# Kernel tuning notes

Hardware: AMD Instinct MI355X
Metric: run time of the kernel (lower is better)

The kernel has to match this reference:

```python
import jax, jax.numpy as jnp
import numpy as np

K = 10
EPS = 1e-5  # BatchNorm eps, eval mode with running_mean=0, running_var=1


def mish(x):
    return x * jnp.tanh(jax.nn.softplus(x))


def knn_idx(x, k):
    # x: (B, C, N); returns (B, N, k) indices of k nearest neighbors (incl. self)
    xx = jnp.sum(x * x, axis=1)                      # (B, N)
    inner = jnp.einsum('bcn,bcm->bnm', x, x)         # (B, N, N)
    neg_d = 2.0 * inner - xx[:, :, None] - xx[:, None, :]
    return jax.lax.top_k(neg_d, k)[1]


def graph_feature(x, k):
    # x: (B, C, N) -> edge features (B, 2C, N, k): cat(nbr - x, x)
    idx = knn_idx(x, k)
    x_t = jnp.transpose(x, (0, 2, 1))                # (B, N, C)
    nbr = jax.vmap(lambda xt, ix: xt[ix])(x_t, idx)  # (B, N, k, C)
    ctr = jnp.broadcast_to(x_t[:, :, None, :], nbr.shape)
    edge = jnp.concatenate([nbr - ctr, ctr], axis=-1)
    return jnp.transpose(edge, (0, 3, 1, 2))


def block2d(x, W, g, b):
    # Conv2d(kernel=1, bias=False) + BatchNorm2d(eval) + Mish
    y = jnp.einsum('oi,bink->bonk', W, x)
    y = y * (g / jnp.sqrt(1.0 + EPS))[None, :, None, None] + b[None, :, None, None]
    return mish(y)


def block1d(x, W, g, b):
    # Conv1d(kernel=1, bias=False) + BatchNorm1d(eval) + Mish
    y = jnp.einsum('oi,bin->bon', W, x)
    y = y * (g / jnp.sqrt(1.0 + EPS))[None, :, None] + b[None, :, None]
    return mish(y)


def setup_inputs() -> dict:
    key = jax.random.key(0)
    ks = jax.random.split(key, 32)
    B, N = 8, 4096
    x = jax.random.normal(ks[0], (B, 3, N), dtype=jnp.float32)

    def w(k, o, i):
        return jax.random.normal(k, (o, i), dtype=jnp.float32) * np.float32(np.sqrt(2.0 / i))

    W1 = w(ks[1], 64, 6)
    W2 = w(ks[2], 64, 128)
    W3 = w(ks[3], 128, 128)
    W4 = w(ks[4], 128, 128)
    W5 = w(ks[5], 128, 256)
    W6 = w(ks[6], 64, 128)
    W7 = w(ks[7], 64, 128)
    W8 = w(ks[8], 64, 128)
    W9 = w(ks[9], 2, 64)

    bn_sizes = [64, 64, 128, 128, 128, 64, 64, 64]
    gs, bs = [], []
    for i, c in enumerate(bn_sizes):
        gs.append(1.0 + 0.1 * jax.random.normal(ks[10 + i], (c,), dtype=jnp.float32))
        bs.append(0.1 * jax.random.normal(ks[20 + i], (c,), dtype=jnp.float32))

    d = {'x': x, 'W1': W1, 'W2': W2, 'W3': W3, 'W4': W4, 'W5': W5,
         'W6': W6, 'W7': W7, 'W8': W8, 'W9': W9}
    for i in range(8):
        d['g%d' % (i + 1)] = gs[i]
        d['b%d' % (i + 1)] = bs[i]
    return d


def reference(x, W1, W2, W3, W4, W5, W6, W7, W8, W9,
              g1, g2, g3, g4, g5, g6, g7, g8,
              b1, b2, b3, b4, b5, b6, b7, b8):
    e = graph_feature(x, K)                      # (B, 6, N, k)
    x1 = jnp.max(block2d(e, W1, g1, b1), axis=-1)  # (B, 64, N)
    e = graph_feature(x1, K)                     # (B, 128, N, k)
    x2 = jnp.max(block2d(e, W2, g2, b2), axis=-1)  # (B, 64, N)
    e = graph_feature(x2, K)                     # (B, 128, N, k)
    x3 = jnp.max(block2d(e, W3, g3, b3), axis=-1)  # (B, 128, N)
    h = block1d(x3, W4, g4, b4)                  # (B, 128, N)
    h = block1d(jnp.concatenate([h, x3], axis=1), W5, g5, b5)  # (B, 128, N)
    h = block1d(h, W6, g6, b6)                   # (B, 64, N)
    h = block1d(jnp.concatenate([h, x2], axis=1), W7, g7, b7)  # (B, 64, N)
    h = block1d(jnp.concatenate([h, x1], axis=1), W8, g8, b8)  # (B, 64, N)
    return jnp.einsum('oi,bin->bon', W9, h)      # (B, 2, N)
```

## Files before the change

kernel.cpp:

```cpp
#include <hip/hip_runtime.h>
#include <hip/hip_bf16.h>
#include <math.h>
#include <float.h>

#define B_ 8
#define N_ 4096
#define M_ (B_*N_)
#define KNN 10

typedef unsigned long long ull;
typedef __attribute__((ext_vector_type(8))) short s16x8;
typedef __attribute__((ext_vector_type(4))) float f32x4;

__device__ __forceinline__ float mishf(float x){
  float sp = (x > 20.f) ? x : __logf(1.f + __expf(x));
  float e2 = __expf(-2.f*sp);
  float th = (1.f - e2) / (1.f + e2);
  return x * th;
}

__device__ __forceinline__ ull shfl_xor_u64(ull v, int mask){
  unsigned lo = (unsigned)v, hi = (unsigned)(v >> 32);
  lo = (unsigned)__shfl_xor((int)lo, mask);
  hi = (unsigned)__shfl_xor((int)hi, mask);
  return ((ull)hi << 32) | lo;
}
__device__ __forceinline__ ull shfl_u64(ull v, int src){
  unsigned lo = (unsigned)v, hi = (unsigned)(v >> 32);
  lo = (unsigned)__shfl((int)lo, src);
  hi = (unsigned)__shfl((int)hi, src);
  return ((ull)hi << 32) | lo;
}
__device__ __forceinline__ int mbcnt_lt(ull mask){
  return __builtin_amdgcn_mbcnt_hi((unsigned)(mask>>32),
         __builtin_amdgcn_mbcnt_lo((unsigned)mask, 0));
}
__device__ __forceinline__ unsigned mono_u32(float f){
  unsigned u = __float_as_uint(f);
  return u ^ ((unsigned)((int)u >> 31) | 0x80000000u);
}
__device__ __forceinline__ float unmono(unsigned vk){
  unsigned u = (vk & 0x80000000u) ? (vk ^ 0x80000000u) : ~vk;
  return __uint_as_float(u);
}
__device__ __forceinline__ void gload_lds16(const void* g, void* l){
  __builtin_amdgcn_global_load_lds(
      (const __attribute__((address_space(1))) unsigned int*)g,
      (__attribute__((address_space(3))) unsigned int*)l, 16, 0, 0);
}

__global__ __launch_bounds__(256) void k_transpose_x(const float* __restrict__ x,
                                                     float* __restrict__ xp){
  int n = blockIdx.x*256 + threadIdx.x;
  if (n >= M_) return;
  int b = n >> 12, i = n & (N_-1);
  const float* xb = x + (size_t)b*3*N_;
  float v0 = xb[i], v1 = xb[N_+i], v2 = xb[2*N_+i];
  float* o = xp + (size_t)n*3;
  o[0]=v0; o[1]=v1; o[2]=v2;
}

template<int C>
__global__ __launch_bounds__(256) void k_xx(const float* __restrict__ X,
                                            float* __restrict__ xx){
  int n = blockIdx.x*256 + threadIdx.x;
  if (n >= M_) return;
  const float* r = X + (size_t)n*C;
  float s = 0.f;
#pragma unroll
  for (int c=0;c<C;c++){ float v=r[c]; s = fmaf(v,v,s); }
  xx[n] = s;
}

__global__ __launch_bounds__(256) void k_cvt(const float* __restrict__ X,
                                             ushort* __restrict__ Xhi,
                                             ushort* __restrict__ Xlo){
  int i = blockIdx.x*256 + threadIdx.x;
  const float4* src = (const float4*)X + (size_t)i*2;
  float4 v0 = src[0], v1 = src[1];
  float vv[8] = {v0.x,v0.y,v0.z,v0.w,v1.x,v1.y,v1.z,v1.w};
  ushort h[8], l[8];
#pragma unroll
  for (int e=0;e<8;e++){
    __hip_bfloat16 hb = __float2bfloat16(vv[e]);
    float hf = __bfloat162float(hb);
    __hip_bfloat16 lb = __float2bfloat16(vv[e]-hf);
    h[e] = *(ushort*)&hb; l[e] = *(ushort*)&lb;
  }
  uint4 hp, lp;
  hp.x = (unsigned)h[0] | ((unsigned)h[1]<<16);
  hp.y = (unsigned)h[2] | ((unsigned)h[3]<<16);
  hp.z = (unsigned)h[4] | ((unsigned)h[5]<<16);
  hp.w = (unsigned)h[6] | ((unsigned)h[7]<<16);
  lp.x = (unsigned)l[0] | ((unsigned)l[1]<<16);
  lp.y = (unsigned)l[2] | ((unsigned)l[3]<<16);
  lp.z = (unsigned)l[4] | ((unsigned)l[5]<<16);
  lp.w = (unsigned)l[6] | ((unsigned)l[7]<<16);
  *(uint4*)(Xhi + (size_t)i*8) = hp;
  *(uint4*)(Xlo + (size_t)i*8) = lp;
}

__global__ __launch_bounds__(256,2) void k_knn64m(const ushort* __restrict__ Xhi,
                                                  const ushort* __restrict__ Xlo,
                                                  const float* __restrict__ xx,
                                                  int* __restrict__ idxout){
  constexpr int JT  = 128;
  constexpr int NT  = N_/JT;
  constexpr int CAP = 320;
  __shared__ ushort XJhi[2][JT*64];
  __shared__ ushort XJlo[2][JT*64];
  __shared__ float  halfxx[2][JT];
  __shared__ ull    buf[4][CAP];

  const int t    = threadIdx.x;
  const int w    = t >> 6;
  const int lane = t & 63;
  const int b    = blockIdx.x & 7;
  const int i0   = (blockIdx.x >> 3) * 64;
  const size_t rowbase = (size_t)b*N_;
  const float* xxb = xx + rowbase;

  const int arow = i0 + w*16 + (lane & 15);
  const ushort* Ah = Xhi + (rowbase + arow)*64;
  const ushort* Al = Xlo + (rowbase + arow)*64;
  const int ko = (lane >> 4)*8;
  s16x8 aH0 = *(const s16x8*)(Ah + ko);
  s16x8 aH1 = *(const s16x8*)(Ah + 32 + ko);
  s16x8 aL0 = *(const s16x8*)(Al + ko);
  s16x8 aL1 = *(const s16x8*)(Al + 32 + ko);

  ull kq[KNN];
#pragma unroll
  for (int q=0;q<KNN;q++) kq[q]=0ull;
  float Treg = -INFINITY;

  const int lr = lane >> 3;
  const int sc = (lane & 7) ^ lr;

  {
#pragma unroll
    for (int seg=0; seg<4; ++seg){
      const int row0 = w*32 + seg*8;
      gload_lds16(Xhi + (rowbase + row0 + lr)*64 + sc*8, &XJhi[0][row0*64]);
      gload_lds16(Xlo + (rowbase + row0 + lr)*64 + sc*8, &XJlo[0][row0*64]);
    }
    if (t < JT) halfxx[0][t] = 0.5f*xxb[t];
  }
  __syncthreads();

  for (int jt = 0; jt < NT; ++jt){
    const int cur = jt & 1;
    const int j0 = jt*JT;

    float hnext = 0.f;
    if (jt < NT-1){
      const size_t nb0 = rowbase + j0 + JT;
#pragma unroll
      for (int seg=0; seg<4; ++seg){
        const int row0 = w*32 + seg*8;
        gload_lds16(Xhi + (nb0 + row0 + lr)*64 + sc*8, &XJhi[cur^1][row0*64]);
        gload_lds16(Xlo + (nb0 + row0 + lr)*64 + sc*8, &XJlo[cur^1][row0*64]);
      }
      if (t < JT) hnext = 0.5f*xxb[j0 + JT + t];
    }

    f32x4 acc[8];
#pragma unroll
    for (int cb=0;cb<8;cb++) acc[cb] = (f32x4){0.f,0.f,0.f,0.f};

#pragma unroll
    for (int cb=0;cb<8;cb++){
      const int brow = cb*16 + (lane & 15);
      const unsigned sw = ((unsigned)(brow & 7)) << 4;
      const char* ph = (const char*)&XJhi[cur][0] + brow*128;
      const char* pl = (const char*)&XJlo[cur][0] + brow*128;
      const int kb0 = (int)((unsigned)((lane>>4)<<4) ^ sw);
      const int kb1 = (int)((unsigned)(64 | ((lane>>4)<<4)) ^ sw);
      s16x8 bh0 = *(const s16x8*)(ph + kb0);
      s16x8 bl0 = *(const s16x8*)(pl + kb0);
      s16x8 bh1 = *(const s16x8*)(ph + kb1);
      s16x8 bl1 = *(const s16x8*)(pl + kb1);
      f32x4 a = acc[cb];
      a = __builtin_amdgcn_mfma_f32_16x16x32_bf16(aH0, bh0, a, 0,0,0);
      a = __builtin_amdgcn_mfma_f32_16x16x32_bf16(aH0, bl0, a, 0,0,0);
      a = __builtin_amdgcn_mfma_f32_16x16x32_bf16(aL0, bh0, a, 0,0,0);
      a = __builtin_amdgcn_mfma_f32_16x16x32_bf16(aL0, bl0, a, 0,0,0);
      a = __builtin_amdgcn_mfma_f32_16x16x32_bf16(aH1, bh1, a, 0,0,0);
      a = __builtin_amdgcn_mfma_f32_16x16x32_bf16(aH1, bl1, a, 0,0,0);
      a = __builtin_amdgcn_mfma_f32_16x16x32_bf16(aL1, bh1, a, 0,0,0);
      a = __builtin_amdgcn_mfma_f32_16x16x32_bf16(aL1, bl1, a, 0,0,0);
      acc[cb] = a;
    }

    float hx[8];
#pragma unroll
    for (int cb=0;cb<8;cb++) hx[cb] = halfxx[cur][cb*16 + (lane & 15)];

    if (jt < NT-1 && t < JT) halfxx[cur^1][t] = hnext;

    if (jt == 0){
#pragma unroll
      for (int reg=0;reg<4;reg++){
        const unsigned rl = (unsigned)((lane>>4)*4 + reg);
        ull k8[8];
#pragma unroll
        for (int cb=0;cb<8;cb++){
          float v = acc[cb][reg] - hx[cb];
          unsigned jinv = 4095u - (unsigned)(cb*16 + (lane & 15));
          k8[cb] = ((ull)mono_u32(v)<<32) | ((ull)jinv<<4) | rl;
        }
#pragma unroll
        for (int q=0;q<KNN;q++){
          ull m = k8[0];
#pragma unroll
          for (int s=1;s<8;s++) m = m > k8[s] ? m : k8[s];
          ull v1 = shfl_xor_u64(m,1); m = m>v1?m:v1;
          ull v2 = shfl_xor_u64(m,2); m = m>v2?m:v2;
          ull v4 = shfl_xor_u64(m,4); m = m>v4?m:v4;
          ull v8 = shfl_xor_u64(m,8); m = m>v8?m:v8;
          ull mv = shfl_u64(m, (lane>>2)<<4);
          if (lane < 16 && (lane&3)==reg) kq[q] = mv;
#pragma unroll
          for (int s=0;s<8;s++) k8[s] = (k8[s]==m) ? 0ull : k8[s];
        }
      }
      Treg = unmono((unsigned)(kq[KNN-1] >> 32));
    } else {
      float Tf[4];
#pragma unroll
      for (int reg=0;reg<4;reg++) Tf[reg] = __shfl(Treg, (lane>>4)*4 + reg);
      int cnt = 0;
#pragma unroll
      for (int cb=0;cb<8;cb++){
#pragma unroll
        for (int reg=0;reg<4;reg++){
          float v = acc[cb][reg] - hx[cb];
          bool pass = v >= Tf[reg];
          ull mask = __ballot(pass);
          if (mask){
            if (pass){
              int slot = cnt + mbcnt_lt(mask);
              unsigned jinv = 4095u - (unsigned)(j0 + cb*16 + (lane & 15));
              ull key = ((ull)mono_u32(v)<<32) | ((ull)jinv<<4)
                        | (unsigned)((lane>>4)*4 + reg);
              if (slot < CAP) buf[w][slot] = key;
            }
            cnt += __popcll(mask);
          }
        }
      }
      if (cnt){
        int nb = cnt < CAP ? cnt : CAP;
        int pad = (4 - (nb & 3)) & 3;
        if (lane < pad && nb + lane < CAP) buf[w][nb + lane] = 0ull;
        int nb4 = nb + pad; if (nb4 > CAP) nb4 = CAP;
        for (int e=0;e<nb4;e+=4){
          ull c0=buf[w][e+0], c1=buf[w][e+1], c2=buf[w][e+2], c3=buf[w][e+3];
#pragma unroll
          for (int u=0;u<4;u++){
            ull k64 = (u==0)?c0:(u==1)?c1:(u==2)?c2:c3;
            if ((int)(k64 & 15ull) == lane && k64 > kq[KNN-1]){
              ull ck = k64;
#pragma unroll
              for (int q=0;q<KNN;q++){
                ull hi = ck > kq[q] ? ck : kq[q];
                ull lo = ck > kq[q] ? kq[q] : ck;
                kq[q] = hi; ck = lo;
              }
            }
          }
        }
        Treg = unmono((unsigned)(kq[KNN-1] >> 32));
      }
    }
    __syncthreads();
  }

  if (lane < 16){
    int* o = idxout + ((size_t)b*N_ + i0 + w*16 + lane)*KNN;
#pragma unroll
    for (int q=0;q<KNN;q++) o[q] = (int)(4095u - (unsigned)((kq[q]>>4) & 4095ull));
  }
}

template<int C>
__global__ __launch_bounds__(256,2) void k_knn(const float* __restrict__ X,
                                               const float* __restrict__ xx,
                                               int* __restrict__ idxout){
  constexpr bool BIG = (C % 4 == 0);
  constexpr int LS  = BIG ? (C + 4) : 12;
  constexpr int NC4 = BIG ? (C/4 + 1) : 1;
  constexpr int JT  = 128;
  constexpr int CAP = 320;
  __shared__ float XI[64*LS];
  __shared__ float XJ[JT*LS];
  __shared__ ull   buf[4][CAP];

  const int t    = threadIdx.x;
  const int w    = t >> 6;
  const int lane = t & 63;
  const int b    = blockIdx.y;
  const int i0   = blockIdx.x*64;
  const int tc   = t & 15, tr = t >> 4;
  const float* Xb  = X  + (size_t)b*N_*C;
  const float* xxb = xx + (size_t)b*N_;

  if constexpr (BIG){
    for (int f = t; f < 64*(C/4); f += 256){
      int r = f >> 4, c4 = f & 15;
      *(float4*)&XI[r*LS + c4*4] = *(const float4*)&Xb[(size_t)(i0+r)*C + c4*4];
    }
    if (t < 64){ XI[t*LS+C]=1.f; XI[t*LS+C+1]=0.f; XI[t*LS+C+2]=0.f; XI[t*LS+C+3]=0.f; }
  } else {
    if (t < 64){
      const float* p = &Xb[(size_t)(i0+t)*C];
      XI[t*LS+0]=p[0]; XI[t*LS+1]=p[1]; XI[t*LS+2]=p[2]; XI[t*LS+3]=1.f;
    }
  }

  ull kq[KNN];
#pragma unroll
  for (int q=0;q<KNN;q++) kq[q]=0ull;
  float Treg = -INFINITY;

  for (int jt = 0; jt < N_/JT; ++jt){
    const int j0 = jt*JT;
    if constexpr (BIG){
      for (int f = t; f < JT*(C/4); f += 256){
        int r = f >> 4, c4 = f & 15;
        *(float4*)&XJ[r*LS + c4*4] = *(const float4*)&Xb[(size_t)(j0+r)*C + c4*4];
      }
      if (t < JT){ XJ[t*LS+C] = -0.5f*xxb[j0+t]; XJ[t*LS+C+1]=0.f; XJ[t*LS+C+2]=0.f; XJ[t*LS+C+3]=0.f; }
    } else {
      if (t < JT){
        const float* p = &Xb[(size_t)(j0+t)*C];
        XJ[t*LS+0]=p[0]; XJ[t*LS+1]=p[1]; XJ[t*LS+2]=p[2]; XJ[t*LS+3]=-0.5f*xxb[j0+t];
      }
    }
    __syncthreads();

    float acc[4][8];
#pragma unroll
    for (int rr=0;rr<4;rr++)
#pragma unroll
      for (int s=0;s<8;s++) acc[rr][s]=0.f;

#pragma unroll 2
    for (int c4 = 0; c4 < NC4; ++c4){
      float4 xi0 = *(const float4*)&XI[(tr*4+0)*LS + c4*4];
      float4 xi1 = *(const float4*)&XI[(tr*4+1)*LS + c4*4];
      float4 xi2 = *(const float4*)&XI[(tr*4+2)*LS + c4*4];
      float4 xi3 = *(const float4*)&XI[(tr*4+3)*LS + c4*4];
#pragma unroll
      for (int s=0;s<8;s++){
        float4 xj = *(const float4*)&XJ[(tc+16*s)*LS + c4*4];
        float a0=acc[0][s], a1=acc[1][s], a2=acc[2][s], a3=acc[3][s];
        a0=fmaf(xi0.x,xj.x,a0); a1=fmaf(xi1.x,xj.x,a1); a2=fmaf(xi2.x,xj.x,a2); a3=fmaf(xi3.x,xj.x,a3);
        a0=fmaf(xi0.y,xj.y,a0); a1=fmaf(xi1.y,xj.y,a1); a2=fmaf(xi2.y,xj.y,a2); a3=fmaf(xi3.y,xj.y,a3);
        a0=fmaf(xi0.z,xj.z,a0); a1=fmaf(xi1.z,xj.z,a1); a2=fmaf(xi2.z,xj.z,a2); a3=fmaf(xi3.z,xj.z,a3);
        a0=fmaf(xi0.w,xj.w,a0); a1=fmaf(xi1.w,xj.w,a1); a2=fmaf(xi2.w,xj.w,a2); a3=fmaf(xi3.w,xj.w,a3);
        acc[0][s]=a0; acc[1][s]=a1; acc[2][s]=a2; acc[3][s]=a3;
      }
    }

    if (jt == 0){
#pragma unroll
      for (int rr=0;rr<4;rr++){
        const unsigned rl = (unsigned)((lane>>4)*4 + rr);
        ull k8[8];
#pragma unroll
        for (int s=0;s<8;s++){
          unsigned jinv = 4095u - (unsigned)(tc + 16*s);
          k8[s] = ((ull)mono_u32(acc[rr][s])<<32) | ((ull)jinv<<4) | rl;
        }
#pragma unroll
        for (int q=0;q<KNN;q++){
          ull m = k8[0];
#pragma unroll
          for (int s=1;s<8;s++) m = m > k8[s] ? m : k8[s];
          ull v1 = shfl_xor_u64(m,1); m = m>v1?m:v1;
          ull v2 = shfl_xor_u64(m,2); m = m>v2?m:v2;
          ull v4 = shfl_xor_u64(m,4); m = m>v4?m:v4;
          ull v8 = shfl_xor_u64(m,8); m = m>v8?m:v8;
          ull mv = shfl_u64(m, (lane>>2)<<4);
          if (lane < 16 && (lane&3)==rr) kq[q] = mv;
#pragma unroll
          for (int s=0;s<8;s++) k8[s] = (k8[s]==m) ? 0ull : k8[s];
        }
      }
      Treg = unmono((unsigned)(kq[KNN-1] >> 32));
    } else {
      float Tf[4];
#pragma unroll
      for (int rr=0;rr<4;rr++) Tf[rr] = __shfl(Treg, (lane>>4)*4 + rr);
      int cnt = 0;
#pragma unroll
      for (int s=0;s<8;s++){
#pragma unroll
        for (int rr=0;rr<4;rr++){
          bool pass = acc[rr][s] >= Tf[rr];
          ull mask = __ballot(pass);
          if (mask){
            if (pass){
              int slot = cnt + mbcnt_lt(mask);
              unsigned jinv = 4095u - (unsigned)(j0 + tc + 16*s);
              ull key = ((ull)mono_u32(acc[rr][s])<<32) | ((ull)jinv<<4)
                        | (unsigned)((lane>>4)*4 + rr);
              if (slot < CAP) buf[w][slot] = key;
            }
            cnt += __popcll(mask);
          }
        }
      }
      if (cnt){
        int nb = cnt < CAP ? cnt : CAP;
        for (int e=0;e<nb;e++){
          ull k64 = buf[w][e];
          if ((int)(k64 & 15ull) == lane && k64 > kq[KNN-1]){
            ull ck = k64;
#pragma unroll
            for (int q=0;q<KNN;q++){
              ull hi = ck > kq[q] ? ck : kq[q];
              ull lo = ck > kq[q] ? kq[q] : ck;
              kq[q] = hi; ck = lo;
            }
          }
        }
        Treg = unmono((unsigned)(kq[KNN-1] >> 32));
      }
    }
    __syncthreads();
  }

  if (lane < 16){
    int* o = idxout + ((size_t)b*N_ + i0 + w*16 + lane)*KNN;
#pragma unroll
    for (int q=0;q<KNN;q++) o[q] = (int)(4095u - (unsigned)((kq[q]>>4) & 4095ull));
  }
}

template<int PT>
__global__ __launch_bounds__(256) void k_gemm(
    const float* __restrict__ X1, int C1,
    const float* __restrict__ X2, int C2,
    const float* __restrict__ W, int hmask, int hshift, int wstride, int hoff,
    const float* __restrict__ g, const float* __restrict__ bb, int act,
    float* __restrict__ Y, int Pfull)
{
  constexpr int CPT = PT/16;
  constexpr int WLS = PT + 4;
  __shared__ float Xt[32*68];
  __shared__ float Wt[32*WLS];
  const int t  = threadIdx.x;
  const int r0 = blockIdx.x*64;
  const int p0 = blockIdx.y*PT;
  const int cg = t & 15, rg = t >> 4;
  const int C = C1 + C2;
  const int nkt = (C + 31) >> 5;

  float acc[4][CPT];
#pragma unroll
  for (int a=0;a<4;a++)
#pragma unroll
    for (int c=0;c<CPT;c++) acc[a][c]=0.f;

  for (int kt = 0; kt < nkt; ++kt){
    const int k0 = kt*32;
#pragma unroll
    for (int e = t; e < 64*32; e += 256){
      int kk = e & 31, r = e >> 5;
      int gk = k0 + kk;
      float v = 0.f;
      if (gk < C1) v = X1[(size_t)(r0+r)*C1 + gk];
      else if (gk < C) v = X2[(size_t)(r0+r)*C2 + (gk - C1)];
      Xt[kk*68 + r] = v;
    }
#pragma unroll
    for (int e = t; e < PT*32; e += 256){
      int kk = e & 31, p = e >> 5;
      int gp = p0 + p;
      int wrow = (gp & hmask)*wstride + (gp >> hshift)*hoff;
      int gk = k0 + kk;
      Wt[kk*WLS + p] = (gk < C) ? W[(size_t)wrow + gk] : 0.f;
    }
    __syncthreads();
#pragma unroll
    for (int kk=0;kk<32;kk++){
      float4 xv = *(const float4*)&Xt[kk*68 + rg*4];
      float xr[4] = {xv.x, xv.y, xv.z, xv.w};
      float wv[CPT];
#pragma unroll
      for (int c4=0;c4<CPT/4;c4++){
        float4 w4 = *(const float4*)&Wt[kk*WLS + cg*CPT + c4*4];
        wv[c4*4+0]=w4.x; wv[c4*4+1]=w4.y; wv[c4*4+2]=w4.z; wv[c4*4+3]=w4.w;
      }
#pragma unroll
      for (int rr=0;rr<4;rr++)
#pragma unroll
        for (int cc=0;cc<CPT;cc++)
          acc[rr][cc] = fmaf(xr[rr], wv[cc], acc[rr][cc]);
    }
    __syncthreads();
  }

  const float srs = rsqrtf(1.f + 1e-5f);
  float sv[CPT], bvv[CPT];
#pragma unroll
  for (int cc=0;cc<CPT;cc++){
    int gp = p0 + cg*CPT + cc;
    if (g){ sv[cc] = g[gp]*srs; bvv[cc] = bb[gp]; } else { sv[cc]=1.f; bvv[cc]=0.f; }
  }
#pragma unroll
  for (int rr=0;rr<4;rr++){
    size_t row = r0 + rg*4 + rr;
    float* yr = Y + row*(size_t)Pfull + p0 + cg*CPT;
#pragma unroll
    for (int c4=0;c4<CPT/4;c4++){
      float y0 = sv[c4*4+0]*acc[rr][c4*4+0] + bvv[c4*4+0];
      float y1 = sv[c4*4+1]*acc[rr][c4*4+1] + bvv[c4*4+1];
      float y2 = sv[c4*4+2]*acc[rr][c4*4+2] + bvv[c4*4+2];
      float y3 = sv[c4*4+3]*acc[rr][c4*4+3] + bvv[c4*4+3];
      if (act){ y0=mishf(y0); y1=mishf(y1); y2=mishf(y2); y3=mishf(y3); }
      *(float4*)&yr[c4*4] = make_float4(y0,y1,y2,y3);
    }
  }
}

template<int O>
__global__ __launch_bounds__(256) void k_edgemax(
    const float* __restrict__ ua, const int* __restrict__ idx,
    const float* __restrict__ g, const float* __restrict__ bb,
    float* __restrict__ Y)
{
  constexpr int TPR = O/4;
  const int gt = blockIdx.x*256 + threadIdx.x;
  const int m  = gt / TPR;
  const int og = gt % TPR;
  if (m >= M_) return;
  const int base = m & ~(N_-1);
  const int P = 2*O;
  const float4 u0 = *(const float4*)&ua[(size_t)m*P + og*4];
  const float4 a0 = *(const float4*)&ua[(size_t)m*P + O + og*4];
  const float srs = rsqrtf(1.f + 1e-5f);
  const float4 gv  = *(const float4*)&g[og*4];
  const float4 bv4 = *(const float4*)&bb[og*4];
  const float sx = gv.x*srs, sy = gv.y*srs, sz = gv.z*srs, sw = gv.w*srs;
  const float cx = a0.x - u0.x, cy = a0.y - u0.y, cz = a0.z - u0.z, cw = a0.w - u0.w;
  float mx = -INFINITY, my = -INFINITY, mz = -INFINITY, mw = -INFINITY;
  const int* id = idx + (size_t)m*KNN;
#pragma unroll
  for (int k=0;k<KNN;k++){
    int j = id[k];
    const float4 uj = *(const float4*)&ua[(size_t)(base + j)*P + og*4];
    float zx = fmaf(sx, uj.x + cx, bv4.x);
    float zy = fmaf(sy, uj.y + cy, bv4.y);
    float zz = fmaf(sz, uj.z + cz, bv4.z);
    float zw = fmaf(sw, uj.w + cw, bv4.w);
    mx = fmaxf(mx, mishf(zx));
    my = fmaxf(my, mishf(zy));
    mz = fmaxf(mz, mishf(zz));
    mw = fmaxf(mw, mishf(zw));
  }
  *(float4*)&Y[(size_t)m*O + og*4] = make_float4(mx,my,mz,mw);
}

__global__ __launch_bounds__(256) void k_final(const float* __restrict__ h,
                                               const float* __restrict__ W9,
                                               float* __restrict__ out){
  __shared__ float w[128];
  const int t = threadIdx.x;
  if (t < 128) w[t] = W9[t];
  __syncthreads();
  const int m = blockIdx.x*256 + t;
  if (m >= M_) return;
  const int b = m >> 12, i = m & (N_-1);
  const float* hr = h + (size_t)m*64;
  float s0 = 0.f, s1 = 0.f;
#pragma unroll
  for (int c=0;c<64;c++){ float v = hr[c]; s0 = fmaf(w[c], v, s0); s1 = fmaf(w[64+c], v, s1); }
  out[((size_t)b*2 + 0)*N_ + i] = s0;
  out[((size_t)b*2 + 1)*N_ + i] = s1;
}

extern "C" void kernel_launch(void* const* d_in, const int* in_sizes, int n_in,
                              void* d_out, int out_size, void* d_ws, size_t ws_size,
                              hipStream_t stream)
{
  const float* x  = (const float*)d_in[0];
  const float* W1 = (const float*)d_in[1];
  const float* W2 = (const float*)d_in[2];
  const float* W3 = (const float*)d_in[3];
  const float* W4 = (const float*)d_in[4];
  const float* W5 = (const float*)d_in[5];
  const float* W6 = (const float*)d_in[6];
  const float* W7 = (const float*)d_in[7];
  const float* W8 = (const float*)d_in[8];
  const float* W9 = (const float*)d_in[9];
  const float* g1 = (const float*)d_in[10]; const float* b1 = (const float*)d_in[11];
  const float* g2 = (const float*)d_in[12]; const float* b2 = (const float*)d_in[13];
  const float* g3 = (const float*)d_in[14]; const float* b3 = (const float*)d_in[15];
  const float* g4 = (const float*)d_in[16]; const float* b4 = (const float*)d_in[17];
  const float* g5 = (const float*)d_in[18]; const float* b5 = (const float*)d_in[19];
  const float* g6 = (const float*)d_in[20]; const float* b6 = (const float*)d_in[21];
  const float* g7 = (const float*)d_in[22]; const float* b7 = (const float*)d_in[23];
  const float* g8 = (const float*)d_in[24]; const float* b8 = (const float*)d_in[25];
  float* out = (float*)d_out;

  float* ws  = (float*)d_ws;
  float* xp  = ws;
  float* xx  = xp + 98304;
  int*   idx = (int*)(xx + 32768);
  float* ua  = (float*)(idx + 327680);
  float* x1  = ua + 8388608;
  float* x2  = x1 + 2097152;
  float* x3  = x2 + 2097152;
  float* h4  = x3 + 4194304;
  float* h5  = h4 + 4194304;
  float* h6  = x3;
  float* h7  = h4;
  float* h8  = h5;
  ushort* Xhi = (ushort*)ua;
  ushort* Xlo = (ushort*)(ua + 1048576);

  const dim3 blk(256);
  const float* nullf = nullptr;

  k_transpose_x<<<dim3(M_/256), blk, 0, stream>>>(x, xp);
  k_xx<3><<<dim3(M_/256), blk, 0, stream>>>(xp, xx);
  k_knn<3><<<dim3(N_/64, B_), blk, 0, stream>>>(xp, xx, idx);
  k_gemm<128><<<dim3(M_/64, 1), blk, 0, stream>>>(xp, 3, nullf, 0,
      W1, 63, 6, 6, 3, nullf, nullf, 0, ua, 128);
  k_edgemax<64><<<dim3(M_*16/256), blk, 0, stream>>>(ua, idx, g1, b1, x1);

  k_xx<64><<<dim3(M_/256), blk, 0, stream>>>(x1, xx);
  k_cvt<<<dim3(M_*64/(8*256)), blk, 0, stream>>>(x1, Xhi, Xlo);
  k_knn64m<<<dim3(512), blk, 0, stream>>>(Xhi, Xlo, xx, idx);
  k_gemm<128><<<dim3(M_/64, 1), blk, 0, stream>>>(x1, 64, nullf, 0,
      W2, 63, 6, 128, 64, nullf, nullf, 0, ua, 128);
  k_edgemax<64><<<dim3(M_*16/256), blk, 0, stream>>>(ua, idx, g2, b2, x2);

  k_xx<64><<<dim3(M_/256), blk, 0, stream>>>(x2, xx);
  k_cvt<<<dim3(M_*64/(8*256)), blk, 0, stream>>>(x2, Xhi, Xlo);
  k_knn64m<<<dim3(512), blk, 0, stream>>>(Xhi, Xlo, xx, idx);
  k_gemm<128><<<dim3(M_/64, 2), blk, 0, stream>>>(x2, 64, nullf, 0,
      W3, 127, 7, 128, 64, nullf, nullf, 0, ua, 256);
  k_edgemax<128><<<dim3(M_*32/256), blk, 0, stream>>>(ua, idx, g3, b3, x3);

  k_gemm<128><<<dim3(M_/64, 1), blk, 0, stream>>>(x3, 128, nullf, 0,
      W4, 127, 7, 128, 0, g4, b4, 1, h4, 128);
  k_gemm<128><<<dim3(M_/64, 1), blk, 0, stream>>>(h4, 128, x3, 128,
      W5, 127, 7, 256, 0, g5, b5, 1, h5, 128);
  k_gemm<64><<<dim3(M_/64, 1), blk, 0, stream>>>(h5, 128, nullf, 0,
      W6, 63, 6, 128, 0, g6, b6, 1, h6, 64);
  k_gemm<64><<<dim3(M_/64, 1), blk, 0, stream>>>(h6, 64, x2, 64,
      W7, 63, 6, 128, 0, g7, b7, 1, h7, 64);
  k_gemm<64><<<dim3(M_/64, 1), blk, 0, stream>>>(h7, 64, x1, 64,
      W8, 63, 6, 128, 0, g8, b8, 1, h8, 64);
  k_final<<<dim3(M_/256), blk, 0, stream>>>(h8, W9, out);
}
```

Measured before the change: 1.489 ms.

## Replace 3-channel kNN with per-thread scalar top-k over split candidate halves

The first kNN stage (C=3) no longer uses the tiled LDS kernel. Each thread now owns one query row and scans half of the candidates directly from a packed float4 array (xyz plus -0.5*|x|^2), keeping a register top-10. A small merge kernel then combines the two halves. The packed array is written by the transpose kernel, which removes the separate k_xx launch and the LDS and ballot machinery for this tiny-channel case. The trade-off is a grid of only 256 blocks, an extra merge pass, and per-thread branchy insertion that can diverge within a wavefront.

Measured after the change: 1.593 ms. +7.0%, slower.

```diff
diff --git a/kernel.cpp b/kernel.cpp
--- a/kernel.cpp
+++ b/kernel.cpp
@@ -50,7 +50,8 @@
 }
 
 __global__ __launch_bounds__(256) void k_transpose_x(const float* __restrict__ x,
-                                                     float* __restrict__ xp){
+                                                     float* __restrict__ xp,
+                                                     float4* __restrict__ xp4){
   int n = blockIdx.x*256 + threadIdx.x;
   if (n >= M_) return;
   int b = n >> 12, i = n & (N_-1);
@@ -58,6 +59,8 @@
   float v0 = xb[i], v1 = xb[N_+i], v2 = xb[2*N_+i];
   float* o = xp + (size_t)n*3;
   o[0]=v0; o[1]=v1; o[2]=v2;
+  float s = fmaf(v0,v0,0.f); s = fmaf(v1,v1,s); s = fmaf(v2,v2,s);
+  xp4[n] = make_float4(v0, v1, v2, -0.5f*s);
 }
 
 template<int C>
@@ -98,6 +101,71 @@
   lp.w = (unsigned)l[6] | ((unsigned)l[7]<<16);
   *(uint4*)(Xhi + (size_t)i*8) = hp;
   *(uint4*)(Xlo + (size_t)i*8) = lp;
+}
+
+__global__ __launch_bounds__(256) void k_knn3s(const float4* __restrict__ xp4,
+                                               ull* __restrict__ part){
+  const int bid   = blockIdx.x;
+  const int piece = bid & 1;
+  const int rg    = (bid >> 1) & 15;
+  const int b     = bid >> 5;
+  const int t     = threadIdx.x;
+  const int row   = rg*256 + t;
+  const float4 xi = xp4[(size_t)b*N_ + row];
+  const float4* xj = xp4 + (size_t)b*N_ + piece*2048;
+  const int jbase = piece*2048;
+
+  ull kq[KNN];
+#pragma unroll
+  for (int q=0;q<KNN;q++) kq[q] = 0x007FFFFF00000000ull;
+  float T = -INFINITY;
+
+  for (int jc=0; jc<2048; jc+=8){
+    float4 c[8];
+#pragma unroll
+    for (int u=0;u<8;u++) c[u] = xj[jc+u];
+#pragma unroll
+    for (int u=0;u<8;u++){
+      float a = fmaf(xi.x, c[u].x, 0.f);
+      a = fmaf(xi.y, c[u].y, a);
+      a = fmaf(xi.z, c[u].z, a);
+      float v = a + c[u].w;
+      if (v > T){
+        unsigned jinv = 4095u - (unsigned)(jbase + jc + u);
+        ull ck = ((ull)mono_u32(v)<<32) | jinv;
+#pragma unroll
+        for (int q=0;q<KNN;q++){
+          ull hi = ck > kq[q] ? ck : kq[q];
+          ull lo = ck > kq[q] ? kq[q] : ck;
+          kq[q] = hi; ck = lo;
+        }
+        T = unmono((unsigned)(kq[KNN-1] >> 32));
+      }
+    }
+  }
+
+  ull* o = part + ((size_t)((b*N_ + row)*2 + piece))*KNN;
+#pragma unroll
+  for (int q=0;q<KNN;q++) o[q] = kq[q];
+}
+
+__global__ __launch_bounds__(256) void k_knnmerge(const ull* __restrict__ part,
+                                                  int* __restrict__ idxout){
+  int row = blockIdx.x*256 + threadIdx.x;
+  if (row >= M_) return;
+  const ull* pa = part + (size_t)row*2*KNN;
+  const ull* pb = pa + KNN;
+  int ia=0, ib=0;
+  int* o = idxout + (size_t)row*KNN;
+#pragma unroll
+  for (int s=0;s<KNN;s++){
+    ull ka = (ia < KNN) ? pa[ia] : 0ull;
+    ull kb = (ib < KNN) ? pb[ib] : 0ull;
+    bool ta = ka > kb;
+    ull k = ta ? ka : kb;
+    o[s] = (int)(4095u - ((unsigned)k & 4095u));
+    ia += ta ? 1 : 0; ib += ta ? 0 : 1;
+  }
 }
 
 __global__ __launch_bounds__(256,2) void k_knn64m(const ushort* __restrict__ Xhi,
@@ -283,162 +351,6 @@
   }
 }
 
-template<int C>
-__global__ __launch_bounds__(256,2) void k_knn(const float* __restrict__ X,
-                                               const float* __restrict__ xx,
-                                               int* __restrict__ idxout){
-  constexpr bool BIG = (C % 4 == 0);
-  constexpr int LS  = BIG ? (C + 4) : 12;
-  constexpr int NC4 = BIG ? (C/4 + 1) : 1;
-  constexpr int JT  = 128;
-  constexpr int CAP = 320;
-  __shared__ float XI[64*LS];
-  __shared__ float XJ[JT*LS];
-  __shared__ ull   buf[4][CAP];
-
-  const int t    = threadIdx.x;
-  const int w    = t >> 6;
-  const int lane = t & 63;
-  const int b    = blockIdx.y;
-  const int i0   = blockIdx.x*64;
-  const int tc   = t & 15, tr = t >> 4;
-  const float* Xb  = X  + (size_t)b*N_*C;
-  const float* xxb = xx + (size_t)b*N_;
-
-  if constexpr (BIG){
-    for (int f = t; f < 64*(C/4); f += 256){
-      int r = f >> 4, c4 = f & 15;
-      *(float4*)&XI[r*LS + c4*4] = *(const float4*)&Xb[(size_t)(i0+r)*C + c4*4];
-    }
-    if (t < 64){ XI[t*LS+C]=1.f; XI[t*LS+C+1]=0.f; XI[t*LS+C+2]=0.f; XI[t*LS+C+3]=0.f; }
-  } else {
-    if (t < 64){
-      const float* p = &Xb[(size_t)(i0+t)*C];
-      XI[t*LS+0]=p[0]; XI[t*LS+1]=p[1]; XI[t*LS+2]=p[2]; XI[t*LS+3]=1.f;
-    }
-  }
-
-  ull kq[KNN];
-#pragma unroll
-  for (int q=0;q<KNN;q++) kq[q]=0ull;
-  float Treg = -INFINITY;
-
-  for (int jt = 0; jt < N_/JT; ++jt){
-    const int j0 = jt*JT;
-    if constexpr (BIG){
-      for (int f = t; f < JT*(C/4); f += 256){
-        int r = f >> 4, c4 = f & 15;
-        *(float4*)&XJ[r*LS + c4*4] = *(const float4*)&Xb[(size_t)(j0+r)*C + c4*4];
-      }
-      if (t < JT){ XJ[t*LS+C] = -0.5f*xxb[j0+t]; XJ[t*LS+C+1]=0.f; XJ[t*LS+C+2]=0.f; XJ[t*LS+C+3]=0.f; }
-    } else {
-      if (t < JT){
-        const float* p = &Xb[(size_t)(j0+t)*C];
-        XJ[t*LS+0]=p[0]; XJ[t*LS+1]=p[1]; XJ[t*LS+2]=p[2]; XJ[t*LS+3]=-0.5f*xxb[j0+t];
-      }
-    }
-    __syncthreads();
-
-    float acc[4][8];
-#pragma unroll
-    for (int rr=0;rr<4;rr++)
-#pragma unroll
-      for (int s=0;s<8;s++) acc[rr][s]=0.f;
-
-#pragma unroll 2
-    for (int c4 = 0; c4 < NC4; ++c4){
-      float4 xi0 = *(const float4*)&XI[(tr*4+0)*LS + c4*4];
-      float4 xi1 = *(const float4*)&XI[(tr*4+1)*LS + c4*4];
-      float4 xi2 = *(const float4*)&XI[(tr*4+2)*LS + c4*4];
-      float4 xi3 = *(const float4*)&XI[(tr*4+3)*LS + c4*4];
-#pragma unroll
-      for (int s=0;s<8;s++){
-        float4 xj = *(const float4*)&XJ[(tc+16*s)*LS + c4*4];
-        float a0=acc[0][s], a1=acc[1][s], a2=acc[2][s], a3=acc[3][s];
-        a0=fmaf(xi0.x,xj.x,a0); a1=fmaf(xi1.x,xj.x,a1); a2=fmaf(xi2.x,xj.x,a2); a3=fmaf(xi3.x,xj.x,a3);
-        a0=fmaf(xi0.y,xj.y,a0); a1=fmaf(xi1.y,xj.y,a1); a2=fmaf(xi2.y,xj.y,a2); a3=fmaf(xi3.y,xj.y,a3);
-        a0=fmaf(xi0.z,xj.z,a0); a1=fmaf(xi1.z,xj.z,a1); a2=fmaf(xi2.z,xj.z,a2); a3=fmaf(xi3.z,xj.z,a3);
-        a0=fmaf(xi0.w,xj.w,a0); a1=fmaf(xi1.w,xj.w,a1); a2=fmaf(xi2.w,xj.w,a2); a3=fmaf(xi3.w,xj.w,a3);
-        acc[0][s]=a0; acc[1][s]=a1; acc[2][s]=a2; acc[3][s]=a3;
-      }
-    }
-
-    if (jt == 0){
-#pragma unroll
-      for (int rr=0;rr<4;rr++){
-        const unsigned rl = (unsigned)((lane>>4)*4 + rr);
-        ull k8[8];
-#pragma unroll
-        for (int s=0;s<8;s++){
-          unsigned jinv = 4095u - (unsigned)(tc + 16*s);
-          k8[s] = ((ull)mono_u32(acc[rr][s])<<32) | ((ull)jinv<<4) | rl;
-        }
-#pragma unroll
-        for (int q=0;q<KNN;q++){
-          ull m = k8[0];
-#pragma unroll
-          for (int s=1;s<8;s++) m = m > k8[s] ? m : k8[s];
-          ull v1 = shfl_xor_u64(m,1); m = m>v1?m:v1;
-          ull v2 = shfl_xor_u64(m,2); m = m>v2?m:v2;
-          ull v4 = shfl_xor_u64(m,4); m = m>v4?m:v4;
-          ull v8 = shfl_xor_u64(m,8); m = m>v8?m:v8;
-          ull mv = shfl_u64(m, (lane>>2)<<4);
-          if (lane < 16 && (lane&3)==rr) kq[q] = mv;
-#pragma unroll
-          for (int s=0;s<8;s++) k8[s] = (k8[s]==m) ? 0ull : k8[s];
-        }
-      }
-      Treg = unmono((unsigned)(kq[KNN-1] >> 32));
-    } else {
-      float Tf[4];
-#pragma unroll
-      for (int rr=0;rr<4;rr++) Tf[rr] = __shfl(Treg, (lane>>4)*4 + rr);
-      int cnt = 0;
-#pragma unroll
-      for (int s=0;s<8;s++){
-#pragma unroll
-        for (int rr=0;rr<4;rr++){
-          bool pass = acc[rr][s] >= Tf[rr];
-          ull mask = __ballot(pass);
-          if (mask){
-            if (pass){
-              int slot = cnt + mbcnt_lt(mask);
-              unsigned jinv = 4095u - (unsigned)(j0 + tc + 16*s);
-              ull key = ((ull)mono_u32(acc[rr][s])<<32) | ((ull)jinv<<4)
-                        | (unsigned)((lane>>4)*4 + rr);
-              if (slot < CAP) buf[w][slot] = key;
-            }
-            cnt += __popcll(mask);
-          }
-        }
-      }
-      if (cnt){
-        int nb = cnt < CAP ? cnt : CAP;
-        for (int e=0;e<nb;e++){
-          ull k64 = buf[w][e];
-          if ((int)(k64 & 15ull) == lane && k64 > kq[KNN-1]){
-            ull ck = k64;
-#pragma unroll
-            for (int q=0;q<KNN;q++){
-              ull hi = ck > kq[q] ? ck : kq[q];
-              ull lo = ck > kq[q] ? kq[q] : ck;
-              kq[q] = hi; ck = lo;
-            }
-          }
-        }
-        Treg = unmono((unsigned)(kq[KNN-1] >> 32));
-      }
-    }
-    __syncthreads();
-  }
-
-  if (lane < 16){
-    int* o = idxout + ((size_t)b*N_ + i0 + w*16 + lane)*KNN;
-#pragma unroll
-    for (int q=0;q<KNN;q++) o[q] = (int)(4095u - (unsigned)((kq[q]>>4) & 4095ull));
-  }
-}
-
 template<int PT>
 __global__ __launch_bounds__(256) void k_gemm(
     const float* __restrict__ X1, int C1,
@@ -609,7 +521,8 @@
   float* ws  = (float*)d_ws;
   float* xp  = ws;
   float* xx  = xp + 98304;
-  int*   idx = (int*)(xx + 32768);
+  float4* xp4 = (float4*)(xx + 32768);
+  int*   idx = (int*)(xx + 32768 + 131072);
   float* ua  = (float*)(idx + 327680);
   float* x1  = ua + 8388608;
   float* x2  = x1 + 2097152;
@@ -621,13 +534,14 @@
   float* h8  = h5;
   ushort* Xhi = (ushort*)ua;
   ushort* Xlo = (ushort*)(ua + 1048576);
+  ull*    part = (ull*)(ua + 2097152);
 
   const dim3 blk(256);
   const float* nullf = nullptr;
 
-  k_transpose_x<<<dim3(M_/256), blk, 0, stream>>>(x, xp);
-  k_xx<3><<<dim3(M_/256), blk, 0, stream>>>(xp, xx);
-  k_knn<3><<<dim3(N_/64, B_), blk, 0, stream>>>(xp, xx, idx);
+  k_transpose_x<<<dim3(M_/256), blk, 0, stream>>>(x, xp, xp4);
+  k_knn3s<<<dim3(256), blk, 0, stream>>>(xp4, part);
+  k_knnmerge<<<dim3(M_/256), blk, 0, stream>>>(part, idx);
   k_gemm<128><<<dim3(M_/64, 1), blk, 0, stream>>>(xp, 3, nullf, 0,
       W1, 63, 6, 6, 3, nullf, nullf, 0, ua, 128);
   k_edgemax<64><<<dim3(M_*16/256), blk, 0, stream>>>(ua, idx, g1, b1, x1);
```
